# Performance work log

Measured on AMD Instinct MI355X. Metric: run time of the kernel, lower is better.

The kernel has to match this reference:

```python
import jax, jax.numpy as jnp
import numpy as np

B, S, D = 2, 2048, 1024
H, HD = 16, 64  # num_heads, head_dim; H*HD == D


def setup_inputs() -> dict:
    key = jax.random.key(0)
    ks = jax.random.split(key, 10)
    scale = 1.0 / np.sqrt(D)
    inputs_q = jax.random.normal(ks[0], (B, S, D), dtype=jnp.float32)
    inputs_kv = inputs_q  # self-attention
    Wq = jax.random.normal(ks[1], (D, H, HD), dtype=jnp.float32) * scale
    Wk = jax.random.normal(ks[2], (D, H, HD), dtype=jnp.float32) * scale
    Wv = jax.random.normal(ks[3], (D, H, HD), dtype=jnp.float32) * scale
    Wo = jax.random.normal(ks[4], (H, HD, D), dtype=jnp.float32) * scale
    bq = jnp.zeros((H, HD), dtype=jnp.float32)
    bk = jnp.zeros((H, HD), dtype=jnp.float32)
    bv = jnp.zeros((H, HD), dtype=jnp.float32)
    bo = jnp.zeros((D,), dtype=jnp.float32)
    return {"inputs_q": inputs_q, "inputs_kv": inputs_kv,
            "Wq": Wq, "bq": bq, "Wk": Wk, "bk": bk,
            "Wv": Wv, "bv": bv, "Wo": Wo, "bo": bo}


def reference(inputs_q, inputs_kv, Wq, bq, Wk, bk, Wv, bv, Wo, bo):
    # QKV projections: [B,S,D] x [D,H,HD] -> [B,S,H,HD]
    q = jnp.einsum('bsd,dhe->bshe', inputs_q, Wq) + bq
    k = jnp.einsum('bsd,dhe->bshe', inputs_kv, Wk) + bk
    v = jnp.einsum('bsd,dhe->bshe', inputs_kv, Wv) + bv
    # scale query by sqrt(depth) as in dot_product_attention
    q = q / jnp.sqrt(jnp.asarray(HD, dtype=q.dtype))
    # attention scores: [B,H,Sq,Sk]
    scores = jnp.einsum('bqhd,bkhd->bhqk', q, k)
    weights = jax.nn.softmax(scores, axis=-1)
    # weighted values: [B,Sq,H,HD]
    ctx = jnp.einsum('bhqk,bkhd->bqhd', weights, v)
    # output projection over (head, head_dim) axes
    out = jnp.einsum('bqhd,hde->bqe', ctx, Wo) + bo
    return out
```

## Files before the change

### kernel.cpp

```cpp
#include <hip/hip_runtime.h>
#include <hip/hip_bf16.h>

typedef __bf16 bf16x8 __attribute__((ext_vector_type(8)));
typedef __bf16 bf16x4 __attribute__((ext_vector_type(4)));
typedef float f32x4 __attribute__((ext_vector_type(4)));

#define MFMA(a,b,c) __builtin_amdgcn_mfma_f32_16x16x32_bf16(a,b,c,0,0,0)

__device__ __forceinline__ unsigned short f2bf(float f) {
    union { float f; unsigned u; } x; x.f = f;
    unsigned r = x.u + 0x7fffu + ((x.u >> 16) & 1u);
    return (unsigned short)(r >> 16);
}

__device__ __forceinline__ bf16x8 ld8(const unsigned short* p) {
    return *reinterpret_cast<const bf16x8*>(p);
}

__device__ __forceinline__ float exp2_fast(float x) {
    float r; asm("v_exp_f32 %0, %1" : "=v"(r) : "v"(x)); return r;
}

__device__ __forceinline__ unsigned cvt_pk_bf16(float lo, float hi) {
    unsigned r;
    asm("v_cvt_pk_bf16_f32 %0, %1, %2" : "=v"(r) : "v"(lo), "v"(hi));
    return r;
}

__device__ __forceinline__ void stage16(const unsigned short* g, unsigned short* l) {
    __builtin_amdgcn_global_load_lds(
        (const __attribute__((address_space(1))) unsigned int*)(const void*)(g),
        (__attribute__((address_space(3))) unsigned int*)(void*)(l),
        16, 0, 0);
}

__global__ void k_prep(const float* __restrict__ X, unsigned short* __restrict__ Xb,
                       const float* __restrict__ W0, const float* __restrict__ W1,
                       const float* __restrict__ W2, const float* __restrict__ W3,
                       unsigned short* __restrict__ o0, unsigned short* __restrict__ o1,
                       unsigned short* __restrict__ o2, unsigned short* __restrict__ o3) {
    if (blockIdx.x < 1024) {
        int i = blockIdx.x * 256 + threadIdx.x;
        #pragma unroll
        for (int rep = 0; rep < 4; ++rep, i += 262144) {
            float4 v = reinterpret_cast<const float4*>(X)[i];
            ushort4 o;
            o.x = f2bf(v.x); o.y = f2bf(v.y); o.z = f2bf(v.z); o.w = f2bf(v.w);
            reinterpret_cast<ushort4*>(Xb)[i] = o;
        }
        return;
    }
    __shared__ unsigned short tile[64][66];
    const int which = (blockIdx.x - 1024) >> 8;
    const float* in = which == 0 ? W0 : which == 1 ? W1 : which == 2 ? W2 : W3;
    unsigned short* out = which == 0 ? o0 : which == 1 ? o1 : which == 2 ? o2 : o3;
    const int lb = blockIdx.x & 255;
    int t = threadIdx.x;
    int bk = (lb & 15) * 64, bn = (lb >> 4) * 64;
    #pragma unroll
    for (int r = 0; r < 16; ++r) {
        int k = (t >> 6) * 16 + r;
        int n = t & 63;
        tile[n][k] = f2bf(in[(bk + k) * 1024 + bn + n]);
    }
    __syncthreads();
    #pragma unroll
    for (int r = 0; r < 16; ++r) {
        int n = (t >> 6) * 16 + r;
        int k = t & 63;
        out[(bn + n) * 1024 + bk + k] = tile[n][k];
    }
}

template<int EPI>
__global__ __launch_bounds__(256) void k_gemm_s(
    const unsigned short* __restrict__ A,
    const unsigned short* __restrict__ Bt,
    const float* __restrict__ b0, const float* __restrict__ b1,
    const float* __restrict__ b2,
    unsigned short* __restrict__ q_out, unsigned short* __restrict__ k_out,
    unsigned short* __restrict__ v_out, float* __restrict__ f_out,
    int M, int N, int K)
{
    __shared__ __align__(16) unsigned short A_lds[4][128][32];
    __shared__ __align__(16) unsigned short B_lds[4][128][32];

    const int lane = threadIdx.x & 63;
    const int wave = threadIdx.x >> 6;
    const int wr = wave >> 1, wc = wave & 1;
    const int nbm = M >> 7;
    const int nwg = nbm * (N >> 7);
    int blk = blockIdx.x;
    blk = (blk & 7) * (nwg >> 3) + (blk >> 3);
    const int bm = (blk % nbm) << 7;
    const int bn = (blk / nbm) << 7;
    const int g = lane >> 4, r16 = lane & 15;

    const int srow = lane >> 2;
    const int schunk = lane & 3;
    const unsigned short* Asrc = A  + (size_t)(bm + wave * 32 + srow) * K + schunk * 8;
    const unsigned short* Bsrc = Bt + (size_t)(bn + wave * 32 + srow) * K + schunk * 8;

    auto stage = [&](int buf, int k0) {
        #pragma unroll
        for (int j = 0; j < 2; ++j) {
            stage16(Asrc + (size_t)(j * 16) * K + k0, &A_lds[buf][wave * 32 + j * 16][0]);
            stage16(Bsrc + (size_t)(j * 16) * K + k0, &B_lds[buf][wave * 32 + j * 16][0]);
        }
    };

    f32x4 acc[4][4] = {};

    const int nsteps = K >> 5;
    stage(0, 0);
    stage(1, 32);

    for (int t = 0; t < nsteps; ++t) {
        if (t + 2 < nsteps) stage((t + 2) & 3, (t + 2) * 32);
        if (t < nsteps - 2)       asm volatile("s_waitcnt vmcnt(8)" ::: "memory");
        else if (t == nsteps - 2) asm volatile("s_waitcnt vmcnt(4)" ::: "memory");
        else                      asm volatile("s_waitcnt vmcnt(0)" ::: "memory");
        __builtin_amdgcn_s_barrier();
        __builtin_amdgcn_sched_barrier(0);

        const int cur = t & 3;
        bf16x8 a[4], b[4];
        #pragma unroll
        for (int i = 0; i < 4; ++i)
            a[i] = ld8(&A_lds[cur][wr * 64 + i * 16 + r16][g * 8]);
        #pragma unroll
        for (int j = 0; j < 4; ++j)
            b[j] = ld8(&B_lds[cur][wc * 64 + j * 16 + r16][g * 8]);
        #pragma unroll
        for (int i = 0; i < 4; ++i)
            #pragma unroll
            for (int j = 0; j < 4; ++j)
                acc[i][j] = MFMA(a[i], b[j], acc[i][j]);
    }

    const int seg = bn >> 10;
    const float* bias = (EPI == 1) ? b0 : (seg == 0 ? b0 : (seg == 1 ? b1 : b2));
    const float scale = (EPI == 0 && seg == 0) ? 0.18033688011112042f : 1.0f;

    #pragma unroll
    for (int i = 0; i < 4; ++i)
        #pragma unroll
        for (int j = 0; j < 4; ++j) {
            const int mbase = bm + wr * 64 + i * 16 + g * 4;
            const int n = bn + wc * 64 + j * 16 + r16;
            if constexpr (EPI == 1) {
                #pragma unroll
                for (int r = 0; r < 4; ++r)
                    f_out[(size_t)(mbase + r) * N + n] = acc[i][j][r] + b0[n];
            } else {
                const int nl = n & 1023;
                const int h = nl >> 6, e = nl & 63;
                const int b_ = mbase >> 11, s0 = mbase & 2047;
                float vv[4];
                #pragma unroll
                for (int r = 0; r < 4; ++r)
                    vv[r] = (acc[i][j][r] + bias[nl]) * scale;
                if (seg == 2) {
                    bf16x4 pk = { (__bf16)vv[0], (__bf16)vv[1], (__bf16)vv[2], (__bf16)vv[3] };
                    *reinterpret_cast<bf16x4*>(
                        &v_out[(((size_t)(b_ * 16 + h) * 64 + e) * 2048) + s0]) = pk;
                } else {
                    unsigned short* o = (seg == 0) ? q_out : k_out;
                    #pragma unroll
                    for (int r = 0; r < 4; ++r)
                        o[(((size_t)(b_ * 16 + h) * 2048 + (s0 + r)) * 64) + e] = f2bf(vv[r]);
                }
            }
        }
}

__global__ __launch_bounds__(256) void k_attn(
    const unsigned short* __restrict__ Q,
    const unsigned short* __restrict__ Kb,
    const unsigned short* __restrict__ Vt,
    unsigned short* __restrict__ ctx)
{
    __shared__ __align__(16) unsigned short K_lds[2][128][64];
    __shared__ __align__(16) unsigned short V_lds[2][64][128];

    const int lane = threadIdx.x & 63;
    const int wave = threadIdx.x >> 6;
    const int g = lane >> 4, r16 = lane & 15;

    const int blk = blockIdx.x;
    const int x = blk & 7, i = blk >> 3;
    const int bh = x * 4 + (i & 3);
    const int qb = i >> 2;
    const int b = bh >> 4, h = bh & 15;
    const int q0 = qb * 128 + wave * 32;

    const unsigned short* Qp    = Q  + ((size_t)bh * 2048 + q0) * 64;
    const unsigned short* Khead = Kb + (size_t)bh * 2048 * 64;
    const unsigned short* Vhead = Vt + (size_t)bh * 64 * 2048;

    bf16x8 aq[2][2];
    #pragma unroll
    for (int m = 0; m < 2; ++m)
        #pragma unroll
        for (int h2 = 0; h2 < 2; ++h2)
            aq[m][h2] = ld8(Qp + (size_t)(m * 16 + r16) * 64 + h2 * 32 + g * 8);

    bf16x8 ones;
    #pragma unroll
    for (int j = 0; j < 8; ++j) ones[j] = (__bf16)1.0f;

    const int srow = lane >> 3;
    const int vrow4 = lane >> 4;

    auto stage = [&](int buf, int kt) {
        #pragma unroll
        for (int j = 0; j < 4; ++j) {
            const int scK = (lane & 7) ^ (srow & 3) ^ ((j & 1) << 2);
            stage16(Khead + (size_t)(kt + wave * 32 + j * 8 + srow) * 64 + scK * 8,
                    &K_lds[buf][wave * 32 + j * 8][0]);
        }
        #pragma unroll
        for (int j = 0; j < 4; ++j) {
            const int scV = (lane & 15) ^ (j * 4 + vrow4);
            stage16(Vhead + (size_t)(wave * 16 + j * 4 + vrow4) * 2048 + kt + scV * 8,
                    &V_lds[buf][wave * 16 + j * 4][0]);
        }
    };

    f32x4 o[2][4] = {};
    f32x4 sum_acc[2] = {};

    const int krow0 = (r16 >> 2) * 8 + (r16 & 3);
    const int pik = (r16 & 3) | (((r16 >> 2) & 1) << 2);

    stage(0, 0);
    __syncthreads();

    for (int it = 0; it < 16; ++it) {
        const int cur = it & 1;
        if (it + 1 < 16) stage(cur ^ 1, (it + 1) * 128);

        #pragma unroll
        for (int j = 0; j < 4; ++j) {
            f32x4 s[2][2] = {};
            #pragma unroll
            for (int ch = 0; ch < 2; ++ch) {
                const int krow = 32 * j + ch * 4 + krow0;
                bf16x8 bk0 = ld8(&K_lds[cur][krow][((g)     ^ pik) * 8]);
                bf16x8 bk1 = ld8(&K_lds[cur][krow][((4 + g) ^ pik) * 8]);
                #pragma unroll
                for (int m = 0; m < 2; ++m) {
                    s[m][ch] = MFMA(bk0, aq[m][0], s[m][ch]);
                    s[m][ch] = MFMA(bk1, aq[m][1], s[m][ch]);
                }
            }
            bf16x8 bv[4];
            #pragma unroll
            for (int n = 0; n < 4; ++n)
                bv[n] = ld8(&V_lds[cur][n * 16 + r16][((4 * j + g) ^ r16) * 8]);

            #pragma unroll
            for (int m = 0; m < 2; ++m) {
                float p0 = exp2_fast(s[m][0][0]), p1 = exp2_fast(s[m][0][1]);
                float p2 = exp2_fast(s[m][0][2]), p3 = exp2_fast(s[m][0][3]);
                float p4 = exp2_fast(s[m][1][0]), p5 = exp2_fast(s[m][1][1]);
                float p6 = exp2_fast(s[m][1][2]), p7 = exp2_fast(s[m][1][3]);
                union { bf16x8 v; unsigned u[4]; } A;
                A.u[0] = cvt_pk_bf16(p0, p1);
                A.u[1] = cvt_pk_bf16(p2, p3);
                A.u[2] = cvt_pk_bf16(p4, p5);
                A.u[3] = cvt_pk_bf16(p6, p7);
                #pragma unroll
                for (int n = 0; n < 4; ++n)
                    o[m][n] = MFMA(A.v, bv[n], o[m][n]);
                sum_acc[m] = MFMA(A.v, ones, sum_acc[m]);
            }
        }
        __syncthreads();
    }

    #pragma unroll
    for (int m = 0; m < 2; ++m) {
        float inv[4];
        #pragma unroll
        for (int r = 0; r < 4; ++r) inv[r] = 1.0f / sum_acc[m][r];
        #pragma unroll
        for (int n = 0; n < 4; ++n)
            #pragma unroll
            for (int r = 0; r < 4; ++r) {
                int q = q0 + m * 16 + g * 4 + r;
                float v = o[m][n][r] * inv[r];
                ctx[((size_t)(b * 2048 + q)) * 1024 + h * 64 + n * 16 + r16] = f2bf(v);
            }
    }
}

extern "C" void kernel_launch(void* const* d_in, const int* in_sizes, int n_in,
                              void* d_out, int out_size, void* d_ws, size_t ws_size,
                              hipStream_t stream)
{
    const float* xq  = (const float*)d_in[0];
    const float* Wq  = (const float*)d_in[2];
    const float* bq  = (const float*)d_in[3];
    const float* Wk  = (const float*)d_in[4];
    const float* bk  = (const float*)d_in[5];
    const float* Wv  = (const float*)d_in[6];
    const float* bv  = (const float*)d_in[7];
    const float* Wo  = (const float*)d_in[8];
    const float* bo  = (const float*)d_in[9];
    float* out = (float*)d_out;

    char* ws = (char*)d_ws;
    const size_t MB = 1024 * 1024;
    unsigned short* Xb     = (unsigned short*)(ws + 0);
    unsigned short* Wqkvt  = (unsigned short*)(ws + 16 * MB);
    unsigned short* Wot    = (unsigned short*)(ws + 22 * MB);
    unsigned short* Qb     = (unsigned short*)(ws + 24 * MB);
    unsigned short* Kbuf   = (unsigned short*)(ws + 32 * MB);
    unsigned short* Vt     = (unsigned short*)(ws + 40 * MB);
    unsigned short* Ctx    = (unsigned short*)(ws + 48 * MB);

    k_prep<<<2048, 256, 0, stream>>>(xq, Xb, Wq, Wk, Wv, Wo,
                                     Wqkvt, Wqkvt + 1024 * 1024,
                                     Wqkvt + 2 * 1024 * 1024, Wot);

    k_gemm_s<0><<<768, 256, 0, stream>>>(Xb, Wqkvt, bq, bk, bv,
                                         Qb, Kbuf, Vt, nullptr, 4096, 3072, 1024);

    k_attn<<<512, 256, 0, stream>>>(Qb, Kbuf, Vt, Ctx);

    k_gemm_s<1><<<256, 256, 0, stream>>>(Ctx, Wot, bo, bo, bo,
                                         nullptr, nullptr, nullptr, out, 4096, 1024, 1024);
}
```

Measured before the change: 124.7 us.

## Use 256x256 eight-wave tile for QKV GEMM and simplify output GEMM pipeline

The QKV projection GEMM moves to a new 512-thread kernel with 256x256 tiles, 192 workgroups and split-phase prefetching: each K-step stages one half of the next tile while issuing MFMAs, with s_setprio raised around the MFMA blocks. The larger tile raises operand reuse per LDS load and cuts the number of workgroups. The output-projection GEMM is reduced to a plain double-buffered loop with __syncthreads instead of the 4-deep vmcnt pipeline. The 192 workgroups may underfill the MI355X's CUs, and the simpler output GEMM pipeline may expose more memory latency.

```diff
diff --git a/kernel.cpp b/kernel.cpp
--- a/kernel.cpp
+++ b/kernel.cpp
@@ -72,18 +72,129 @@
     }
 }
 
-template<int EPI>
-__global__ __launch_bounds__(256) void k_gemm_s(
+__global__ __launch_bounds__(512) void k_gemm8(
     const unsigned short* __restrict__ A,
     const unsigned short* __restrict__ Bt,
     const float* __restrict__ b0, const float* __restrict__ b1,
     const float* __restrict__ b2,
     unsigned short* __restrict__ q_out, unsigned short* __restrict__ k_out,
-    unsigned short* __restrict__ v_out, float* __restrict__ f_out,
+    unsigned short* __restrict__ v_out)
+{
+    __shared__ __align__(16) unsigned short A_lds[4][256][32];
+    __shared__ __align__(16) unsigned short B_lds[4][256][32];
+
+    const int lane = threadIdx.x & 63;
+    const int w = threadIdx.x >> 6;
+    const int wr = w >> 2, wc = w & 3;
+    const int g = lane >> 4, r16 = lane & 15;
+
+    int blk = blockIdx.x;
+    blk = (blk & 7) * 24 + (blk >> 3);
+    const int bm = (blk % 16) << 8;
+    const int bn = (blk / 16) << 8;
+
+    const int srow = lane >> 2;
+    const int schunk = lane & 3;
+    const unsigned short* Asrc = A  + (size_t)(bm + w * 32 + srow) * 1024 + schunk * 8;
+    const unsigned short* Bsrc = Bt + (size_t)(bn + w * 32 + srow) * 1024 + schunk * 8;
+
+    auto stage_half = [&](int buf, int k0, int j) {
+        stage16(Asrc + (size_t)(j * 16) * 1024 + k0, &A_lds[buf][w * 32 + j * 16][0]);
+        stage16(Bsrc + (size_t)(j * 16) * 1024 + k0, &B_lds[buf][w * 32 + j * 16][0]);
+    };
+
+    f32x4 acc[8][4] = {};
+
+    const int nkt = 32;
+    stage_half(0, 0, 0); stage_half(0, 0, 1);
+    stage_half(1, 32, 0); stage_half(1, 32, 1);
+
+    for (int t = 0; t < nkt; ++t) {
+        if (t + 1 < nkt) asm volatile("s_waitcnt vmcnt(4)" ::: "memory");
+        else             asm volatile("s_waitcnt vmcnt(0)" ::: "memory");
+        __builtin_amdgcn_s_barrier();
+        __builtin_amdgcn_sched_barrier(0);
+
+        const int cur = t & 3;
+        const bool pf = (t + 2 < nkt);
+        const int pbuf = (t + 2) & 3;
+        const int pk0 = (t + 2) * 32;
+
+        if (pf) stage_half(pbuf, pk0, 0);
+        bf16x8 bfr[4];
+        #pragma unroll
+        for (int nn = 0; nn < 4; ++nn)
+            bfr[nn] = ld8(&B_lds[cur][wc * 64 + nn * 16 + r16][g * 8]);
+        {
+            bf16x8 afr[4];
+            #pragma unroll
+            for (int mm = 0; mm < 4; ++mm)
+                afr[mm] = ld8(&A_lds[cur][wr * 128 + mm * 16 + r16][g * 8]);
+            __builtin_amdgcn_s_setprio(1);
+            #pragma unroll
+            for (int mm = 0; mm < 4; ++mm)
+                #pragma unroll
+                for (int nn = 0; nn < 4; ++nn)
+                    acc[mm][nn] = MFMA(afr[mm], bfr[nn], acc[mm][nn]);
+            __builtin_amdgcn_s_setprio(0);
+        }
+        __builtin_amdgcn_s_barrier();
+
+        if (pf) stage_half(pbuf, pk0, 1);
+        {
+            bf16x8 afr[4];
+            #pragma unroll
+            for (int mm = 0; mm < 4; ++mm)
+                afr[mm] = ld8(&A_lds[cur][wr * 128 + (mm + 4) * 16 + r16][g * 8]);
+            __builtin_amdgcn_s_setprio(1);
+            #pragma unroll
+            for (int mm = 0; mm < 4; ++mm)
+                #pragma unroll
+                for (int nn = 0; nn < 4; ++nn)
+                    acc[mm + 4][nn] = MFMA(afr[mm], bfr[nn], acc[mm + 4][nn]);
+            __builtin_amdgcn_s_setprio(0);
+        }
+    }
+
+    const int seg = bn >> 10;
+    const float* bias = (seg == 0) ? b0 : (seg == 1 ? b1 : b2);
+    const float scale = (seg == 0) ? 0.18033688011112042f : 1.0f;
+
+    #pragma unroll
+    for (int mm = 0; mm < 8; ++mm)
+        #pragma unroll
+        for (int nn = 0; nn < 4; ++nn) {
+            const int mbase = bm + wr * 128 + mm * 16 + g * 4;
+            const int n = bn + wc * 64 + nn * 16 + r16;
+            const int nl = n & 1023;
+            const int h = nl >> 6, e = nl & 63;
+            const int b_ = mbase >> 11, s0 = mbase & 2047;
+            float vv[4];
+            #pragma unroll
+            for (int r = 0; r < 4; ++r)
+                vv[r] = (acc[mm][nn][r] + bias[nl]) * scale;
+            if (seg == 2) {
+                bf16x4 pk = { (__bf16)vv[0], (__bf16)vv[1], (__bf16)vv[2], (__bf16)vv[3] };
+                *reinterpret_cast<bf16x4*>(
+                    &v_out[(((size_t)(b_ * 16 + h) * 64 + e) * 2048) + s0]) = pk;
+            } else {
+                unsigned short* o = (seg == 0) ? q_out : k_out;
+                #pragma unroll
+                for (int r = 0; r < 4; ++r)
+                    o[(((size_t)(b_ * 16 + h) * 2048 + (s0 + r)) * 64) + e] = f2bf(vv[r]);
+            }
+        }
+}
+
+__global__ __launch_bounds__(256) void k_gemm_s(
+    const unsigned short* __restrict__ Ab,
+    const unsigned short* __restrict__ Bt,
+    const float* __restrict__ b0,
+    float* __restrict__ f_out,
     int M, int N, int K)
 {
-    __shared__ __align__(16) unsigned short A_lds[4][128][32];
-    __shared__ __align__(16) unsigned short B_lds[4][128][32];
+    __shared__ __align__(16) unsigned short A_lds[2][128][32];
+    __shared__ __align__(16) unsigned short B_lds[2][128][32];
 
     const int lane = threadIdx.x & 63;
     const int wave = threadIdx.x >> 6;
@@ -98,7 +209,7 @@
 
     const int srow = lane >> 2;
     const int schunk = lane & 3;
-    const unsigned short* Asrc = A  + (size_t)(bm + wave * 32 + srow) * K + schunk * 8;
+    const unsigned short* Asrc = Ab + (size_t)(bm + wave * 32 + srow) * K + schunk * 8;
     const unsigned short* Bsrc = Bt + (size_t)(bn + wave * 32 + srow) * K + schunk * 8;
 
     auto stage = [&](int buf, int k0) {
@@ -111,19 +222,14 @@
 
     f32x4 acc[4][4] = {};
 
+    stage(0, 0);
+    __syncthreads();
+
     const int nsteps = K >> 5;
-    stage(0, 0);
-    stage(1, 32);
-
     for (int t = 0; t < nsteps; ++t) {
-        if (t + 2 < nsteps) stage((t + 2) & 3, (t + 2) * 32);
-        if (t < nsteps - 2)       asm volatile("s_waitcnt vmcnt(8)" ::: "memory");
-        else if (t == nsteps - 2) asm volatile("s_waitcnt vmcnt(4)" ::: "memory");
-        else                      asm volatile("s_waitcnt vmcnt(0)" ::: "memory");
-        __builtin_amdgcn_s_barrier();
-        __builtin_amdgcn_sched_barrier(0);
-
-        const int cur = t & 3;
+        const int cur = t & 1;
+        if (t + 1 < nsteps) stage(cur ^ 1, (t + 1) * 32);
+
         bf16x8 a[4], b[4];
         #pragma unroll
         for (int i = 0; i < 4; ++i)
@@ -136,11 +242,8 @@
             #pragma unroll
             for (int j = 0; j < 4; ++j)
                 acc[i][j] = MFMA(a[i], b[j], acc[i][j]);
-    }
-
-    const int seg = bn >> 10;
-    const float* bias = (EPI == 1) ? b0 : (seg == 0 ? b0 : (seg == 1 ? b1 : b2));
-    const float scale = (EPI == 0 && seg == 0) ? 0.18033688011112042f : 1.0f;
+        __syncthreads();
+    }
 
     #pragma unroll
     for (int i = 0; i < 4; ++i)
@@ -148,29 +251,9 @@
         for (int j = 0; j < 4; ++j) {
             const int mbase = bm + wr * 64 + i * 16 + g * 4;
             const int n = bn + wc * 64 + j * 16 + r16;
-            if constexpr (EPI == 1) {
-                #pragma unroll
-                for (int r = 0; r < 4; ++r)
-                    f_out[(size_t)(mbase + r) * N + n] = acc[i][j][r] + b0[n];
-            } else {
-                const int nl = n & 1023;
-                const int h = nl >> 6, e = nl & 63;
-                const int b_ = mbase >> 11, s0 = mbase & 2047;
-                float vv[4];
-                #pragma unroll
-                for (int r = 0; r < 4; ++r)
-                    vv[r] = (acc[i][j][r] + bias[nl]) * scale;
-                if (seg == 2) {
-                    bf16x4 pk = { (__bf16)vv[0], (__bf16)vv[1], (__bf16)vv[2], (__bf16)vv[3] };
-                    *reinterpret_cast<bf16x4*>(
-                        &v_out[(((size_t)(b_ * 16 + h) * 64 + e) * 2048) + s0]) = pk;
-                } else {
-                    unsigned short* o = (seg == 0) ? q_out : k_out;
-                    #pragma unroll
-                    for (int r = 0; r < 4; ++r)
-                        o[(((size_t)(b_ * 16 + h) * 2048 + (s0 + r)) * 64) + e] = f2bf(vv[r]);
-                }
-            }
+            #pragma unroll
+            for (int r = 0; r < 4; ++r)
+                f_out[(size_t)(mbase + r) * N + n] = acc[i][j][r] + b0[n];
         }
 }
 
@@ -324,11 +407,9 @@
                                      Wqkvt, Wqkvt + 1024 * 1024,
                                      Wqkvt + 2 * 1024 * 1024, Wot);
 
-    k_gemm_s<0><<<768, 256, 0, stream>>>(Xb, Wqkvt, bq, bk, bv,
-                                         Qb, Kbuf, Vt, nullptr, 4096, 3072, 1024);
+    k_gemm8<<<192, 512, 0, stream>>>(Xb, Wqkvt, bq, bk, bv, Qb, Kbuf, Vt);
 
     k_attn<<<512, 256, 0, stream>>>(Qb, Kbuf, Vt, Ctx);
 
-    k_gemm_s<1><<<256, 256, 0, stream>>>(Ctx, Wot, bo, bo, bo,
-                                         nullptr, nullptr, nullptr, out, 4096, 1024, 1024);
-}
+    k_gemm_s<<<256, 256, 0, stream>>>(Ctx, Wot, bo, out, 4096, 1024, 1024);
+}
```

After: 129.4 us. +3.7%, slower.
